# Optimization experiments

Measured on AMD Instinct MI355X. Metric: run time of the kernel, lower is better.

Reference implementation:

```python
import jax, jax.numpy as jnp
import numpy as np


def _ln(x, w, b):
    m = x.mean(-1, keepdims=True)
    v = ((x - m) ** 2).mean(-1, keepdims=True)
    return (x - m) / jnp.sqrt(v + 1e-5) * w + b


def setup_inputs() -> dict:
    key = jax.random.key(0)
    ks = jax.random.split(key, 8)
    N, C, H, W = 2, 64, 128, 128
    heads, ksz = 2, 7
    C4 = 4 * C
    p = lambda k, shape: jax.random.normal(k, shape, dtype=jnp.float32) * 0.02
    return {
        "x": jax.random.normal(ks[0], (N, C, H, W), dtype=jnp.float32),
        "qkv_w": p(ks[1], (3 * C, C)),
        "qkv_b": jnp.zeros((3 * C,), jnp.float32),
        "proj_w": p(ks[2], (C, C)),
        "proj_b": jnp.zeros((C,), jnp.float32),
        "rpb": p(ks[3], (heads, 2 * ksz - 1, 2 * ksz - 1)),
        "ln1_w": jnp.ones((C,), jnp.float32),
        "ln1_b": jnp.zeros((C,), jnp.float32),
        "ln2_w": jnp.ones((C,), jnp.float32),
        "ln2_b": jnp.zeros((C,), jnp.float32),
        "fc1_w": p(ks[4], (C4, C)),
        "fc1_b": jnp.zeros((C4,), jnp.float32),
        "fc2_w": p(ks[5], (C, C4)),
        "fc2_b": jnp.zeros((C,), jnp.float32),
    }


def reference(x, qkv_w, qkv_b, proj_w, proj_b, rpb, ln1_w, ln1_b, ln2_w, ln2_b,
              fc1_w, fc1_b, fc2_w, fc2_b):
    N, C, H, W = x.shape
    heads = rpb.shape[0]
    ksz = (rpb.shape[1] + 1) // 2  # kernel size from (2k-1) bias table
    dh = C // heads

    xt = x.transpose(0, 2, 3, 1).reshape(N, H * W, C)  # n (h w) c
    shortcut = xt
    xn = _ln(xt, ln1_w, ln1_b).reshape(N, H, W, C)

    # qkv projection -> (3, N, heads, H, W, dh)
    qkv = (xn @ qkv_w.T + qkv_b).reshape(N, H, W, 3, heads, dh)
    qkv = qkv.transpose(3, 0, 4, 1, 2, 5)
    q = qkv[0] * (dh ** -0.5)
    k = qkv[1]
    v = qkv[2]

    # NATTEN neighborhood: window start clamped so every query sees k x k keys
    sh = jnp.clip(jnp.arange(H) - ksz // 2, 0, H - ksz)
    sw = jnp.clip(jnp.arange(W) - ksz // 2, 0, W - ksz)
    rows = sh[:, None] + jnp.arange(ksz)  # (H, k) key row indices
    cols = sw[:, None] + jnp.arange(ksz)  # (W, k) key col indices

    # relative position bias index: (query - key) + (k-1) in [0, 2k-2]
    rel_h = jnp.arange(H)[:, None] - rows + (ksz - 1)  # (H, k)
    rel_w = jnp.arange(W)[:, None] - cols + (ksz - 1)  # (W, k)
    bias = rpb[:, rel_h][:, :, :, rel_w]               # (heads, H, k, W, k)
    bias = bias.transpose(0, 1, 3, 2, 4)               # (heads, H, W, k, k)

    ri = rows[:, None, :, None]  # (H,1,k,1)
    ci = cols[None, :, None, :]  # (1,W,1,k)
    kwin = k[:, :, ri, ci, :]    # (N, heads, H, W, k, k, dh)
    vwin = v[:, :, ri, ci, :]

    scores = jnp.einsum('nzhwd,nzhwijd->nzhwij', q, kwin) + bias[None]
    attn = jax.nn.softmax(scores.reshape(N, heads, H, W, ksz * ksz), axis=-1)
    out = jnp.einsum('nzhwe,nzhwed->nzhwd', attn,
                     vwin.reshape(N, heads, H, W, ksz * ksz, dh))
    out = out.transpose(0, 2, 3, 1, 4).reshape(N, H, W, C) @ proj_w.T + proj_b

    x2 = shortcut + out.reshape(N, H * W, C)
    y = _ln(x2, ln2_w, ln2_b)
    y = jax.nn.gelu(y @ fc1_w.T + fc1_b, approximate=False) @ fc2_w.T + fc2_b
    x3 = x2 + y
    return x3.reshape(N, H, W, C).transpose(0, 3, 1, 2)
```

## Files before the change

### kernel.cpp

```cpp
#include <hip/hip_runtime.h>
#include <math.h>

#define TQ   32768
#define HWSZ 16384
#define CC   64
#define HH   128
#define WW   128
#define C3   192
#define C4   256
#define KS   7

typedef _Float16 half2v __attribute__((ext_vector_type(2)));
typedef _Float16 half4v __attribute__((ext_vector_type(4)));
typedef _Float16 half8v __attribute__((ext_vector_type(8)));
typedef float    f32x4  __attribute__((ext_vector_type(4)));

#define MFMA16(a, b, c) __builtin_amdgcn_mfma_f32_16x16x32_f16((a), (b), (c), 0, 0, 0)

__device__ __forceinline__ float gelu_f(float v) {
    float z = v * (1.59576912f + 0.07135481f * v * v);
    float e = __expf(-z);
    return v * (1.f / (1.f + e));
}

__global__ __launch_bounds__(256) void k_qkvln(const float* __restrict__ x,
        const float* __restrict__ lnw, const float* __restrict__ lnb,
        const float* __restrict__ qw, const float* __restrict__ qb,
        const float* __restrict__ pw, const float* __restrict__ f1w,
        const float* __restrict__ f2w,
        _Float16* __restrict__ qkv16, _Float16* __restrict__ pw16,
        _Float16* __restrict__ f1w16, _Float16* __restrict__ f2w16) {
    __shared__ union {
        struct { __align__(16) _Float16 A[128 * 72]; __align__(16) _Float16 B[192 * 72]; } st;
        __align__(16) _Float16 outb[128 * 200];
    } u;
    __shared__ float ps1[256], ps2[256], m_s[128], r_s[128];
    __shared__ float w_s[64], b_s[64], bias_s[192];
    int tid = threadIdx.x;
    int t0 = blockIdx.x * 128;
    if (tid < 64) { w_s[tid] = lnw[tid]; b_s[tid] = lnb[tid]; }
    if (tid < 192) bias_s[tid] = qb[tid];
    int tok = tid & 127, cq = tid >> 7;
    int t = t0 + tok;
    int n = t >> 14, hw = t & (HWSZ - 1);
    const float* xr = x + ((size_t)n << 20) + hw;
    float v[32];
    float s = 0.f, s2 = 0.f;
#pragma unroll
    for (int e = 0; e < 32; ++e) {
        float f = xr[(cq * 32 + e) * HWSZ];
        v[e] = f; s += f; s2 += f * f;
    }
    ps1[tid] = s; ps2[tid] = s2;
    for (int i = tid; i < 3072; i += 256) {
        int jj = i >> 4, seg = i & 15;
        float4 v4 = *(const float4*)&qw[(size_t)jj * 64 + seg * 4];
        half4v h4 = { (_Float16)v4.x, (_Float16)v4.y, (_Float16)v4.z, (_Float16)v4.w };
        *(half4v*)&u.st.B[jj * 72 + seg * 4] = h4;
    }
    {
        int g = blockIdx.x * 256 + tid;
        if (g < 4096) pw16[g] = (_Float16)pw[g];
        else if (g < 20480) f1w16[g - 4096] = (_Float16)f1w[g - 4096];
        else if (g < 36864) f2w16[g - 20480] = (_Float16)f2w[g - 20480];
    }
    __syncthreads();
    if (tid < 128) {
        float ss = ps1[tid] + ps1[tid + 128];
        float qq = ps2[tid] + ps2[tid + 128];
        float m = ss * (1.f / 64.f);
        float var = qq * (1.f / 64.f) - m * m;
        m_s[tid] = m; r_s[tid] = rsqrtf(var + 1e-5f);
    }
    __syncthreads();
    {
        float m = m_s[tok], r = r_s[tok];
#pragma unroll
        for (int u8 = 0; u8 < 4; ++u8) {
            half8v o;
#pragma unroll
            for (int e = 0; e < 8; ++e) {
                int c = cq * 32 + u8 * 8 + e;
                o[e] = (_Float16)((v[u8 * 8 + e] - m) * r * w_s[c] + b_s[c]);
            }
            *(half8v*)&u.st.A[tok * 72 + cq * 32 + u8 * 8] = o;
        }
    }
    __syncthreads();
    int lane = tid & 63, wv = tid >> 6;
    int quad = lane >> 4, l16 = lane & 15;
    int mt0 = (wv & 1) * 64, nt0 = (wv >> 1) * 96;
    f32x4 acc[4][6];
#pragma unroll
    for (int mf = 0; mf < 4; ++mf)
#pragma unroll
        for (int nf = 0; nf < 6; ++nf) acc[mf][nf] = (f32x4){0.f, 0.f, 0.f, 0.f};
#pragma unroll
    for (int ks = 0; ks < 64; ks += 32) {
        half8v a[4], bfr[6];
#pragma unroll
        for (int mf = 0; mf < 4; ++mf)
            a[mf] = *(const half8v*)&u.st.A[(mt0 + mf * 16 + l16) * 72 + ks + quad * 8];
#pragma unroll
        for (int nf = 0; nf < 6; ++nf)
            bfr[nf] = *(const half8v*)&u.st.B[(nt0 + nf * 16 + l16) * 72 + ks + quad * 8];
#pragma unroll
        for (int mf = 0; mf < 4; ++mf)
#pragma unroll
            for (int nf = 0; nf < 6; ++nf) acc[mf][nf] = MFMA16(a[mf], bfr[nf], acc[mf][nf]);
    }
    __syncthreads();
    const float qscale = 0.17677669529663687f;
#pragma unroll
    for (int mf = 0; mf < 4; ++mf)
#pragma unroll
        for (int nf = 0; nf < 6; ++nf) {
            int j = nt0 + nf * 16 + l16;
            float bias = bias_s[j];
            float sc = (j < 64) ? qscale : 1.f;
#pragma unroll
            for (int r = 0; r < 4; ++r) {
                int tl = mt0 + mf * 16 + quad * 4 + r;
                u.outb[tl * 200 + j] = (_Float16)((acc[mf][nf][r] + bias) * sc);
            }
        }
    __syncthreads();
    for (int i = tid; i < 4096; i += 256) {
        int tk = i >> 5, rem = i & 31;
        if (rem < 24)
            *(half8v*)&qkv16[(size_t)(t0 + tk) * C3 + rem * 8] =
                *(const half8v*)&u.outb[tk * 200 + rem * 8];
    }
}

__global__ __launch_bounds__(256) void k_attn_mlp(const _Float16* __restrict__ qkv16,
        const float* __restrict__ rpb,
        const _Float16* __restrict__ pw16, const float* __restrict__ pb,
        const float* __restrict__ x,
        const float* __restrict__ ln2w, const float* __restrict__ ln2b,
        const _Float16* __restrict__ f1w16, const float* __restrict__ f1b,
        const _Float16* __restrict__ f2w16, const float* __restrict__ f2b,
        float* __restrict__ out) {
    __shared__ __align__(16) char smem[78216];
    _Float16* kv_s  = (_Float16*)smem;
    _Float16* q_s   = (_Float16*)(smem + 53312);
    _Float16* s_s   = (_Float16*)(smem + 63552);
    float*    rpb_s = (float*)(smem + 76352);
    float*    sum_s = (float*)(smem + 77704);
    float* x2t  = (float*)smem;
    float* ps1  = (float*)(smem + 20480);
    float* ps2  = (float*)(smem + 21504);
    float* m_s  = (float*)(smem + 22528);
    float* r_s  = (float*)(smem + 22784);
    float* w_s  = (float*)(smem + 23040);
    float* b_s  = (float*)(smem + 23296);
    float* pb_s = (float*)(smem + 23552);
    _Float16* A2_s = (_Float16*)(smem + 53312);
    _Float16* H_s  = (_Float16*)(smem + 17408);
    float*    tr_s = (float*)(smem + 17408);
    float*    f1b_s = (float*)(smem + 63552);
    float*    f2b_s = (float*)(smem + 64576);

    int tid = threadIdx.x;
    int bx = blockIdx.x;
    int n  = bx >> 8;
    int th = (bx >> 4) & 15, tw = bx & 15;
    int h0 = th * 8, w0 = tw * 8;
    int wr0 = min(max(h0 - 3, 0), HH - 14);
    int ww0 = min(max(w0 - 3, 0), WW - 14);
    int tbase = n << 14;
    int lane = tid & 63, wvi = tid >> 6;
    int quad = lane >> 4, l16 = lane & 15;

    for (int i = tid; i < 338; i += 256) rpb_s[i] = rpb[i];
    for (int i = tid; i < 196 * 16; i += 256) {
        int tok = i >> 4, u = i & 15;
        int wi = tok / 14, wj = tok - wi * 14;
        *(half8v*)&kv_s[tok * 136 + u * 8] = *(const half8v*)&qkv16[
            (size_t)(tbase + (wr0 + wi) * WW + ww0 + wj) * C3 + 64 + u * 8];
    }
    for (int i = tid; i < 64 * 8; i += 256) {
        int q = i >> 3, u = i & 7;
        int qg = tbase + (h0 + (q >> 3)) * WW + (w0 + (q & 7));
        *(half8v*)&q_s[q * 80 + u * 8] = *(const half8v*)&qkv16[(size_t)qg * C3 + u * 8];
    }
    __syncthreads();

    int c16 = tid & 1, z = (tid >> 1) & 1, q = tid >> 2;
    int qy = q >> 3, qx = q & 7;
    int h = h0 + qy, wc = w0 + qx;
    int sh = min(max(h - 3, 0), HH - KS);
    int sw = min(max(wc - 3, 0), WW - KS);
    int oh = sh - wr0, ow = sw - ww0;
    int dhp = h - sh + 6, dwp = wc - sw + 6;
    {
        const half8v* qp = (const half8v*)&q_s[q * 80 + z * 32];
        half8v q0 = qp[0], q1 = qp[1], q2 = qp[2], q3 = qp[3];
        int i7 = 0, j7 = c16;
        for (int nb = c16; nb < 49; nb += 2) {
            int tok = (oh + i7) * 14 + (ow + j7);
            const half8v* kp = (const half8v*)&kv_s[tok * 136 + z * 32];
            half2v acc2 = { (_Float16)0.f, (_Float16)0.f };
            half8v k0 = kp[0], k1 = kp[1], k2 = kp[2], k3 = kp[3];
            acc2 += (half2v){k0.s0, k0.s1} * (half2v){q0.s0, q0.s1};
            acc2 += (half2v){k0.s2, k0.s3} * (half2v){q0.s2, q0.s3};
            acc2 += (half2v){k0.s4, k0.s5} * (half2v){q0.s4, q0.s5};
            acc2 += (half2v){k0.s6, k0.s7} * (half2v){q0.s6, q0.s7};
            acc2 += (half2v){k1.s0, k1.s1} * (half2v){q1.s0, q1.s1};
            acc2 += (half2v){k1.s2, k1.s3} * (half2v){q1.s2, q1.s3};
            acc2 += (half2v){k1.s4, k1.s5} * (half2v){q1.s4, q1.s5};
            acc2 += (half2v){k1.s6, k1.s7} * (half2v){q1.s6, q1.s7};
            acc2 += (half2v){k2.s0, k2.s1} * (half2v){q2.s0, q2.s1};
            acc2 += (half2v){k2.s2, k2.s3} * (half2v){q2.s2, q2.s3};
            acc2 += (half2v){k2.s4, k2.s5} * (half2v){q2.s4, q2.s5};
            acc2 += (half2v){k2.s6, k2.s7} * (half2v){q2.s6, q2.s7};
            acc2 += (half2v){k3.s0, k3.s1} * (half2v){q3.s0, q3.s1};
            acc2 += (half2v){k3.s2, k3.s3} * (half2v){q3.s2, q3.s3};
            acc2 += (half2v){k3.s4, k3.s5} * (half2v){q3.s4, q3.s5};
            acc2 += (half2v){k3.s6, k3.s7} * (half2v){q3.s6, q3.s7};
            float s = (float)acc2.x + (float)acc2.y
                    + rpb_s[(z * 13 + (dhp - i7)) * 13 + (dwp - j7)];
            s_s[(q * 2 + z) * 50 + nb] = (_Float16)s;
            j7 += 2;
            if (j7 >= 7) { j7 -= 7; ++i7; }
        }
    }
    __syncthreads();

    if (tid < 128) {
        _Float16* sp = &s_s[tid * 50];
        float mx = -1e30f;
        for (int i = 0; i < 49; ++i) mx = fmaxf(mx, (float)sp[i]);
        float sum = 0.f;
        for (int i = 0; i < 49; ++i) {
            float e = __expf((float)sp[i] - mx);
            sum += e;
            sp[i] = (_Float16)e;
        }
        sum_s[tid] = 1.f / sum;
    }
    __syncthreads();

    {
        const _Float16* pp = &s_s[(q * 2 + z) * 50];
        half2v acc[8];
#pragma unroll
        for (int j = 0; j < 8; ++j) acc[j] = (half2v){ (_Float16)0.f, (_Float16)0.f };
        int i7 = 0, j7 = 0;
        for (int nb = 0; nb < 49; ++nb) {
            int tok = (oh + i7) * 14 + (ow + j7);
            _Float16 p = pp[nb];
            half2v p2 = { p, p };
            const half8v* vp = (const half8v*)&kv_s[tok * 136 + 64 + z * 32 + c16 * 16];
            half8v v0 = vp[0], v1 = vp[1];
            acc[0] += (half2v){v0.s0, v0.s1} * p2;
            acc[1] += (half2v){v0.s2, v0.s3} * p2;
            acc[2] += (half2v){v0.s4, v0.s5} * p2;
            acc[3] += (half2v){v0.s6, v0.s7} * p2;
            acc[4] += (half2v){v1.s0, v1.s1} * p2;
            acc[5] += (half2v){v1.s2, v1.s3} * p2;
            acc[6] += (half2v){v1.s4, v1.s5} * p2;
            acc[7] += (half2v){v1.s6, v1.s7} * p2;
            ++j7;
            if (j7 == 7) { j7 = 0; ++i7; }
        }
        float inv = sum_s[q * 2 + z];
        _Float16* op = q_s + q * 72 + z * 32 + c16 * 16;
        half8v o0, o1;
#pragma unroll
        for (int j = 0; j < 4; ++j) {
            o0[2 * j]     = (_Float16)((float)acc[j].x * inv);
            o0[2 * j + 1] = (_Float16)((float)acc[j].y * inv);
            o1[2 * j]     = (_Float16)((float)acc[4 + j].x * inv);
            o1[2 * j + 1] = (_Float16)((float)acc[4 + j].y * inv);
        }
        *(half8v*)op = o0;
        *(half8v*)(op + 8) = o1;
    }
    __syncthreads();
    for (int i = tid; i < 512; i += 256) {
        int jj = i >> 3, c8 = i & 7;
        *(half8v*)&s_s[jj * 72 + c8 * 8] = *(const half8v*)&pw16[jj * 64 + c8 * 8];
    }
    if (tid < 64) { w_s[tid] = ln2w[tid]; b_s[tid] = ln2b[tid]; pb_s[tid] = pb[tid]; }
    __syncthreads();
    {
        int mt0 = wvi * 16;
        f32x4 acc2[4];
#pragma unroll
        for (int nf = 0; nf < 4; ++nf) acc2[nf] = (f32x4){0.f, 0.f, 0.f, 0.f};
#pragma unroll
        for (int ks = 0; ks < 64; ks += 32) {
            half8v a = *(const half8v*)&q_s[(mt0 + l16) * 72 + ks + quad * 8];
            half8v bfr[4];
#pragma unroll
            for (int nf = 0; nf < 4; ++nf)
                bfr[nf] = *(const half8v*)&s_s[(nf * 16 + l16) * 72 + ks + quad * 8];
#pragma unroll
            for (int nf = 0; nf < 4; ++nf) acc2[nf] = MFMA16(a, bfr[nf], acc2[nf]);
        }
        __syncthreads();
        int tl0 = mt0 + quad * 4;
        int hwl = (h0 + (tl0 >> 3)) * WW + w0 + (tl0 & 7);
#pragma unroll
        for (int nf = 0; nf < 4; ++nf) {
            int j = nf * 16 + l16;
            float bias = pb_s[j];
            float4 rx = *(const float4*)&x[((size_t)(n * CC + j) << 14) + hwl];
#pragma unroll
            for (int r = 0; r < 4; ++r)
                x2t[(tl0 + r) * 68 + j] = acc2[nf][r] + bias + ((const float*)&rx)[r];
        }
    }
    f1b_s[tid] = f1b[tid];
    if (tid < 64) f2b_s[tid] = f2b[tid];
    __syncthreads();
    int tok = tid & 63, cq = tid >> 6;
    {
        float s = 0.f, s2 = 0.f;
#pragma unroll
        for (int e = 0; e < 16; ++e) {
            float f = x2t[tok * 68 + cq * 16 + e];
            s += f; s2 += f * f;
        }
        ps1[tid] = s; ps2[tid] = s2;
    }
    __syncthreads();
    if (tid < 64) {
        float ss = ps1[tid] + ps1[64 + tid] + ps1[128 + tid] + ps1[192 + tid];
        float qq = ps2[tid] + ps2[64 + tid] + ps2[128 + tid] + ps2[192 + tid];
        float m = ss * (1.f / 64.f);
        float var = qq * (1.f / 64.f) - m * m;
        m_s[tid] = m; r_s[tid] = rsqrtf(var + 1e-5f);
    }
    __syncthreads();
    {
        float m = m_s[tok], r = r_s[tok];
        half8v nv0, nv1;
#pragma unroll
        for (int e = 0; e < 8; ++e) {
            int c = cq * 16 + e;
            float f = x2t[tok * 68 + c];
            nv0[e] = (_Float16)((f - m) * r * w_s[c] + b_s[c]);
        }
#pragma unroll
        for (int e = 0; e < 8; ++e) {
            int c = cq * 16 + 8 + e;
            float f = x2t[tok * 68 + c];
            nv1[e] = (_Float16)((f - m) * r * w_s[c] + b_s[c]);
        }
        *(half8v*)&A2_s[tok * 72 + cq * 16] = nv0;
        *(half8v*)&A2_s[tok * 72 + cq * 16 + 8] = nv1;
    }
    __syncthreads();
    {
        int nt0 = wvi * 64;
        f32x4 acc[4][4];
#pragma unroll
        for (int mf = 0; mf < 4; ++mf)
#pragma unroll
            for (int nf = 0; nf < 4; ++nf) acc[mf][nf] = (f32x4){0.f, 0.f, 0.f, 0.f};
#pragma unroll
        for (int ks = 0; ks < 64; ks += 32) {
            half8v a[4], bfr[4];
#pragma unroll
            for (int mf = 0; mf < 4; ++mf)
                a[mf] = *(const half8v*)&A2_s[(mf * 16 + l16) * 72 + ks + quad * 8];
#pragma unroll
            for (int nf = 0; nf < 4; ++nf)
                bfr[nf] = *(const half8v*)&f1w16[(size_t)(nt0 + nf * 16 + l16) * 64 + ks + quad * 8];
#pragma unroll
            for (int mf = 0; mf < 4; ++mf)
#pragma unroll
                for (int nf = 0; nf < 4; ++nf) acc[mf][nf] = MFMA16(a[mf], bfr[nf], acc[mf][nf]);
        }
#pragma unroll
        for (int mf = 0; mf < 4; ++mf)
#pragma unroll
            for (int nf = 0; nf < 4; ++nf) {
                int jl = nt0 + nf * 16 + l16;
                float bias = f1b_s[jl];
#pragma unroll
                for (int r = 0; r < 4; ++r) {
                    int tl = mf * 16 + quad * 4 + r;
                    H_s[tl * 264 + jl] = (_Float16)gelu_f(acc[mf][nf][r] + bias);
                }
            }
    }
    __syncthreads();
    {
        int mt = wvi * 16;
        f32x4 acc2[4];
#pragma unroll
        for (int nf = 0; nf < 4; ++nf) acc2[nf] = (f32x4){0.f, 0.f, 0.f, 0.f};
#pragma unroll
        for (int ks = 0; ks < 256; ks += 32) {
            half8v a = *(const half8v*)&H_s[(mt + l16) * 264 + ks + quad * 8];
            half8v bfr[4];
#pragma unroll
            for (int nf = 0; nf < 4; ++nf)
                bfr[nf] = *(const half8v*)&f2w16[(size_t)(nf * 16 + l16) * 256 + ks + quad * 8];
#pragma unroll
            for (int nf = 0; nf < 4; ++nf) acc2[nf] = MFMA16(a, bfr[nf], acc2[nf]);
        }
        __syncthreads();
#pragma unroll
        for (int nf = 0; nf < 4; ++nf) {
            int j = nf * 16 + l16;
            float bias = f2b_s[j];
#pragma unroll
            for (int r = 0; r < 4; ++r) {
                int tl = mt + quad * 4 + r;
                float v = acc2[nf][r] + bias + x2t[tl * 68 + j];
                tr_s[j * 68 + tl] = v;
            }
        }
    }
    __syncthreads();
    for (int i = tid; i < 2048; i += 256) {
        int j = i >> 5, tl = (i & 31) * 2;
        *(float2*)&out[((size_t)(n * CC + j) << 14)
                       + (size_t)((h0 + (tl >> 3)) * WW + w0 + (tl & 7))] =
            *(const float2*)&tr_s[j * 68 + tl];
    }
}

extern "C" void kernel_launch(void* const* d_in, const int* in_sizes, int n_in,
                              void* d_out, int out_size, void* d_ws, size_t ws_size,
                              hipStream_t stream) {
    const float* x      = (const float*)d_in[0];
    const float* qkv_w  = (const float*)d_in[1];
    const float* qkv_b  = (const float*)d_in[2];
    const float* proj_w = (const float*)d_in[3];
    const float* proj_b = (const float*)d_in[4];
    const float* rpb    = (const float*)d_in[5];
    const float* ln1_w  = (const float*)d_in[6];
    const float* ln1_b  = (const float*)d_in[7];
    const float* ln2_w  = (const float*)d_in[8];
    const float* ln2_b  = (const float*)d_in[9];
    const float* fc1_w  = (const float*)d_in[10];
    const float* fc1_b  = (const float*)d_in[11];
    const float* fc2_w  = (const float*)d_in[12];
    const float* fc2_b  = (const float*)d_in[13];
    float* out = (float*)d_out;
    char* ws = (char*)d_ws;

    _Float16* qkv16  = (_Float16*)(ws);
    _Float16* pw16   = (_Float16*)(ws + 20971520);
    _Float16* f1w16  = (_Float16*)(ws + 20979712);
    _Float16* f2w16  = (_Float16*)(ws + 21012480);

    k_qkvln   <<<256, 256, 0, stream>>>(x, ln1_w, ln1_b, qkv_w, qkv_b,
                                        proj_w, fc1_w, fc2_w,
                                        qkv16, pw16, f1w16, f2w16);
    k_attn_mlp<<<512, 256, 0, stream>>>(qkv16, rpb, pw16, proj_b, x, ln2_w, ln2_b,
                                        f1w16, fc1_b, f2w16, fc2_b, out);
}
```

Measured before the change: 125.9 us.

## Halve QKV tile per block, split softmax across thread pairs, prefetch proj weights

```diff
diff --git a/kernel.cpp b/kernel.cpp
--- a/kernel.cpp
+++ b/kernel.cpp
@@ -31,24 +31,24 @@
         _Float16* __restrict__ qkv16, _Float16* __restrict__ pw16,
         _Float16* __restrict__ f1w16, _Float16* __restrict__ f2w16) {
     __shared__ union {
-        struct { __align__(16) _Float16 A[128 * 72]; __align__(16) _Float16 B[192 * 72]; } st;
-        __align__(16) _Float16 outb[128 * 200];
+        struct { __align__(16) _Float16 A[64 * 72]; __align__(16) _Float16 B[192 * 72]; } st;
+        __align__(16) _Float16 outb[64 * 200];
     } u;
-    __shared__ float ps1[256], ps2[256], m_s[128], r_s[128];
+    __shared__ float ps1[256], ps2[256], m_s[64], r_s[64];
     __shared__ float w_s[64], b_s[64], bias_s[192];
     int tid = threadIdx.x;
-    int t0 = blockIdx.x * 128;
+    int t0 = blockIdx.x * 64;
     if (tid < 64) { w_s[tid] = lnw[tid]; b_s[tid] = lnb[tid]; }
     if (tid < 192) bias_s[tid] = qb[tid];
-    int tok = tid & 127, cq = tid >> 7;
+    int tok = tid & 63, cq = tid >> 6;
     int t = t0 + tok;
     int n = t >> 14, hw = t & (HWSZ - 1);
     const float* xr = x + ((size_t)n << 20) + hw;
-    float v[32];
+    float v[16];
     float s = 0.f, s2 = 0.f;
 #pragma unroll
-    for (int e = 0; e < 32; ++e) {
-        float f = xr[(cq * 32 + e) * HWSZ];
+    for (int e = 0; e < 16; ++e) {
+        float f = xr[(cq * 16 + e) * HWSZ];
         v[e] = f; s += f; s2 += f * f;
     }
     ps1[tid] = s; ps2[tid] = s2;
@@ -65,9 +65,9 @@
         else if (g < 36864) f2w16[g - 20480] = (_Float16)f2w[g - 20480];
     }
     __syncthreads();
-    if (tid < 128) {
-        float ss = ps1[tid] + ps1[tid + 128];
-        float qq = ps2[tid] + ps2[tid + 128];
+    if (tid < 64) {
+        float ss = ps1[tid] + ps1[tid + 64] + ps1[tid + 128] + ps1[tid + 192];
+        float qq = ps2[tid] + ps2[tid + 64] + ps2[tid + 128] + ps2[tid + 192];
         float m = ss * (1.f / 64.f);
         float var = qq * (1.f / 64.f) - m * m;
         m_s[tid] = m; r_s[tid] = rsqrtf(var + 1e-5f);
@@ -76,56 +76,56 @@
     {
         float m = m_s[tok], r = r_s[tok];
 #pragma unroll
-        for (int u8 = 0; u8 < 4; ++u8) {
+        for (int u8 = 0; u8 < 2; ++u8) {
             half8v o;
 #pragma unroll
             for (int e = 0; e < 8; ++e) {
-                int c = cq * 32 + u8 * 8 + e;
+                int c = cq * 16 + u8 * 8 + e;
                 o[e] = (_Float16)((v[u8 * 8 + e] - m) * r * w_s[c] + b_s[c]);
             }
-            *(half8v*)&u.st.A[tok * 72 + cq * 32 + u8 * 8] = o;
+            *(half8v*)&u.st.A[tok * 72 + cq * 16 + u8 * 8] = o;
         }
     }
     __syncthreads();
     int lane = tid & 63, wv = tid >> 6;
     int quad = lane >> 4, l16 = lane & 15;
-    int mt0 = (wv & 1) * 64, nt0 = (wv >> 1) * 96;
-    f32x4 acc[4][6];
+    int nt0 = wv * 48;
+    f32x4 acc[4][3];
 #pragma unroll
     for (int mf = 0; mf < 4; ++mf)
 #pragma unroll
-        for (int nf = 0; nf < 6; ++nf) acc[mf][nf] = (f32x4){0.f, 0.f, 0.f, 0.f};
+        for (int nf = 0; nf < 3; ++nf) acc[mf][nf] = (f32x4){0.f, 0.f, 0.f, 0.f};
 #pragma unroll
     for (int ks = 0; ks < 64; ks += 32) {
-        half8v a[4], bfr[6];
+        half8v a[4], bfr[3];
 #pragma unroll
         for (int mf = 0; mf < 4; ++mf)
-            a[mf] = *(const half8v*)&u.st.A[(mt0 + mf * 16 + l16) * 72 + ks + quad * 8];
-#pragma unroll
-        for (int nf = 0; nf < 6; ++nf)
+            a[mf] = *(const half8v*)&u.st.A[(mf * 16 + l16) * 72 + ks + quad * 8];
+#pragma unroll
+        for (int nf = 0; nf < 3; ++nf)
             bfr[nf] = *(const half8v*)&u.st.B[(nt0 + nf * 16 + l16) * 72 + ks + quad * 8];
 #pragma unroll
         for (int mf = 0; mf < 4; ++mf)
 #pragma unroll
-            for (int nf = 0; nf < 6; ++nf) acc[mf][nf] = MFMA16(a[mf], bfr[nf], acc[mf][nf]);
+            for (int nf = 0; nf < 3; ++nf) acc[mf][nf] = MFMA16(a[mf], bfr[nf], acc[mf][nf]);
     }
     __syncthreads();
     const float qscale = 0.17677669529663687f;
 #pragma unroll
     for (int mf = 0; mf < 4; ++mf)
 #pragma unroll
-        for (int nf = 0; nf < 6; ++nf) {
+        for (int nf = 0; nf < 3; ++nf) {
             int j = nt0 + nf * 16 + l16;
             float bias = bias_s[j];
             float sc = (j < 64) ? qscale : 1.f;
 #pragma unroll
             for (int r = 0; r < 4; ++r) {
-                int tl = mt0 + mf * 16 + quad * 4 + r;
+                int tl = mf * 16 + quad * 4 + r;
                 u.outb[tl * 200 + j] = (_Float16)((acc[mf][nf][r] + bias) * sc);
             }
         }
     __syncthreads();
-    for (int i = tid; i < 4096; i += 256) {
+    for (int i = tid; i < 2048; i += 256) {
         int tk = i >> 5, rem = i & 31;
         if (rem < 24)
             *(half8v*)&qkv16[(size_t)(t0 + tk) * C3 + rem * 8] =
@@ -184,6 +184,8 @@
         int qg = tbase + (h0 + (q >> 3)) * WW + (w0 + (q & 7));
         *(half8v*)&q_s[q * 80 + u * 8] = *(const half8v*)&qkv16[(size_t)qg * C3 + u * 8];
     }
+    half8v pwr0 = *(const half8v*)&pw16[(size_t)tid * 8];
+    half8v pwr1 = *(const half8v*)&pw16[(size_t)(tid + 256) * 8];
     __syncthreads();
 
     int c16 = tid & 1, z = (tid >> 1) & 1, q = tid >> 2;
@@ -227,17 +229,21 @@
     }
     __syncthreads();
 
-    if (tid < 128) {
-        _Float16* sp = &s_s[tid * 50];
+    {
+        int row = tid >> 1, h2 = tid & 1;
+        _Float16* sp = &s_s[row * 50];
+        int i0 = h2 ? 25 : 0, i1 = h2 ? 49 : 25;
         float mx = -1e30f;
-        for (int i = 0; i < 49; ++i) mx = fmaxf(mx, (float)sp[i]);
+        for (int i = i0; i < i1; ++i) mx = fmaxf(mx, (float)sp[i]);
+        mx = fmaxf(mx, __shfl_xor(mx, 1));
         float sum = 0.f;
-        for (int i = 0; i < 49; ++i) {
+        for (int i = i0; i < i1; ++i) {
             float e = __expf((float)sp[i] - mx);
             sum += e;
             sp[i] = (_Float16)e;
         }
-        sum_s[tid] = 1.f / sum;
+        sum += __shfl_xor(sum, 1);
+        if (h2 == 0) sum_s[row] = 1.f / sum;
     }
     __syncthreads();
 
@@ -278,9 +284,10 @@
         *(half8v*)(op + 8) = o1;
     }
     __syncthreads();
-    for (int i = tid; i < 512; i += 256) {
-        int jj = i >> 3, c8 = i & 7;
-        *(half8v*)&s_s[jj * 72 + c8 * 8] = *(const half8v*)&pw16[jj * 64 + c8 * 8];
+    {
+        int i0 = tid, i1 = tid + 256;
+        *(half8v*)&s_s[(i0 >> 3) * 72 + (i0 & 7) * 8] = pwr0;
+        *(half8v*)&s_s[(i1 >> 3) * 72 + (i1 & 7) * 8] = pwr1;
     }
     if (tid < 64) { w_s[tid] = ln2w[tid]; b_s[tid] = ln2b[tid]; pb_s[tid] = pb[tid]; }
     __syncthreads();
@@ -450,7 +457,7 @@
     _Float16* f1w16  = (_Float16*)(ws + 20979712);
     _Float16* f2w16  = (_Float16*)(ws + 21012480);
 
-    k_qkvln   <<<256, 256, 0, stream>>>(x, ln1_w, ln1_b, qkv_w, qkv_b,
+    k_qkvln   <<<512, 256, 0, stream>>>(x, ln1_w, ln1_b, qkv_w, qkv_b,
                                         proj_w, fc1_w, fc2_w,
                                         qkv16, pw16, f1w16, f2w16);
     k_attn_mlp<<<512, 256, 0, stream>>>(qkv16, rpb, pw16, proj_b, x, ln2_w, ln2_b,
```

New measurement: 127.8 us. About the same (+1.5%).
